# Kernel optimization log

Measured on AMD Instinct MI355X. Metric: run time of the kernel, lower is better.

Reference implementation:

```python
import jax, jax.numpy as jnp
import numpy as np

NUM_HEADS = 16
D_MODEL = 2048
DUPLICATES = 4
DEPTH = D_MODEL // NUM_HEADS  # 128
KV_HEADS = NUM_HEADS // DUPLICATES  # 4


def rope(x):
    # x: (b, s, d); RoPE over first 2*(d//2) dims (d even here), as in source
    b, s, d = x.shape
    dim = d // 2
    inv_freq = (10000.0 ** (-jnp.arange(0, dim, dtype=jnp.float32) / dim)).astype(x.dtype)
    pos = jnp.arange(s, dtype=x.dtype)[None, :, None]  # (1, s, 1)
    freqs = pos * inv_freq  # (1, s, dim)
    cos, sin = jnp.cos(freqs), jnp.sin(freqs)
    x1, x2 = x[..., :dim], x[..., dim:]
    return jnp.concatenate([x1 * cos - x2 * sin, x2 * cos + x1 * sin], axis=-1)


def setup_inputs() -> dict:
    key = jax.random.key(0)
    ks = jax.random.split(key, 6)
    b, s = 2, 2048
    x = jax.random.normal(ks[0], (b, s, D_MODEL), dtype=jnp.float32)
    mask = jnp.ones((b, 1, s, s), dtype=bool)
    std = 0.02
    Wq = jax.random.normal(ks[1], (D_MODEL, D_MODEL), dtype=jnp.float32) * std
    Wk = jax.random.normal(ks[2], (D_MODEL, D_MODEL // DUPLICATES), dtype=jnp.float32) * std
    Wv = jax.random.normal(ks[3], (D_MODEL, D_MODEL // DUPLICATES), dtype=jnp.float32) * std
    Wo = jax.random.normal(ks[4], (D_MODEL, D_MODEL), dtype=jnp.float32) * std
    bo = jnp.zeros((1, 1, D_MODEL), dtype=jnp.float32)
    return {"x": x, "mask": mask, "Wq": Wq, "Wk": Wk, "Wv": Wv, "Wo": Wo, "bo": bo}


def reference(x, mask, Wq, Wk, Wv, Wo, bo):
    b, s, d = x.shape
    # QKV projections; RoPE applied on full projected vectors (as in source)
    q = rope(x @ Wq)          # (b, s, d_model)
    k = rope(x @ Wk)          # (b, s, d_model/dup)
    v = x @ Wv                # (b, s, d_model/dup)
    # split heads
    q = q.reshape(b, s, NUM_HEADS, DEPTH).transpose(0, 2, 1, 3)     # (b, H, s, depth)
    k = k.reshape(b, s, KV_HEADS, DEPTH).transpose(0, 2, 1, 3)      # (b, Hkv, s, depth)
    v = v.reshape(b, s, KV_HEADS, DEPTH).transpose(0, 2, 1, 3)
    # GQA repeat (jnp.repeat on head axis, matching source)
    k = jnp.repeat(k, DUPLICATES, axis=1)                            # (b, H, s, depth)
    v = jnp.repeat(v, DUPLICATES, axis=1)
    # scaled dot-product attention (chunking in source is a pure partition of q; math identical)
    logits = jnp.einsum('bhqd,bhkd->bhqk', q, k) / jnp.sqrt(jnp.asarray(DEPTH, x.dtype))
    logits = jnp.where(mask, logits, jnp.asarray(-1e9, x.dtype))
    attn = jax.nn.softmax(logits, axis=-1)
    out = jnp.einsum('bhqk,bhkd->bhqd', attn, v)                     # (b, H, s, depth)
    out = out.transpose(0, 2, 1, 3).reshape(b, s, d)
    return out @ Wo + bo
```

## Files before the change

kernel.cpp:

```cpp
#include <hip/hip_runtime.h>
#include <hip/hip_bf16.h>
#include <stdint.h>

#define NHEADS 16
#define KVHEADS 4
#define DEPTH 128
#define SEQ 2048
#define DM 2048
#define NQKV 3072
#define SCALE 0.08838834764831845f

using u16 = unsigned short;
using u32 = unsigned int;
using u64 = unsigned long long;
using bf16x8 = __attribute__((ext_vector_type(8))) __bf16;
using f32x4  = __attribute__((ext_vector_type(4))) float;
using f32x16 = __attribute__((ext_vector_type(16))) float;
using u32x4  = __attribute__((ext_vector_type(4))) u32;

__device__ __forceinline__ u16 bits(float f) {
  return __builtin_bit_cast(u16, (__bf16)f);
}
__device__ __forceinline__ u32 pk2(float a, float b) {
  return (u32)bits(a) | ((u32)bits(b) << 16);
}

__device__ __forceinline__ void gll16(const void* g, void* l) {
  __builtin_amdgcn_global_load_lds((const __attribute__((address_space(1))) void*)g,
                                   (__attribute__((address_space(3))) void*)l, 16, 0, 0);
}


__global__ void k_cvt_x(const float4* __restrict__ x, u16* __restrict__ o, int n4) {
  int i = blockIdx.x * 256 + threadIdx.x;
  if (i >= n4) return;
  float4 v = x[i];
  u64 pk = (u64)bits(v.x) | ((u64)bits(v.y) << 16) | ((u64)bits(v.z) << 32) | ((u64)bits(v.w) << 48);
  reinterpret_cast<u64*>(o)[i] = pk;
}

__global__ void k_transpose_w(const float* __restrict__ in, u16* __restrict__ out, int K, int N) {
  __shared__ float tile[32][33];
  int n0 = blockIdx.x * 32, k0 = blockIdx.y * 32;
  int tx = threadIdx.x, ty = threadIdx.y;
  for (int i = 0; i < 4; i++) tile[ty + i * 8][tx] = in[(size_t)(k0 + ty + i * 8) * N + n0 + tx];
  __syncthreads();
  for (int i = 0; i < 4; i++)
    out[(size_t)(n0 + ty + i * 8) * K + k0 + tx] = bits(tile[tx][ty + i * 8]);
}

__global__ void k_trig(float2* __restrict__ tab) {
  int idx = blockIdx.x * 256 + threadIdx.x;
  int s = idx >> 10, j = idx & 1023;
  float inv = expf((float)j * (-9.210340371976184f / 1024.f));
  float f = (float)s * inv;
  float sv, cv;
  sincosf(f, &sv, &cv);
  tab[idx] = make_float2(cv, sv);
}

__global__ void k_rope_q(const float* __restrict__ qkv, const float2* __restrict__ tab,
                         u16* __restrict__ Qh) {
  int idx = blockIdx.x * 256 + threadIdx.x;
  int col = idx & 2047;
  int row = idx >> 11;
  int s = row & 2047;
  const float* base = qkv + (size_t)row * NQKV;
  float v = base[col], out;
  if (col < 1024) {
    float2 cs = tab[s * 1024 + col];
    out = v * cs.x - base[col + 1024] * cs.y;
  } else {
    int j = col - 1024;
    float2 cs = tab[s * 1024 + j];
    out = v * cs.x + base[col - 1024] * cs.y;
  }
  int h = col >> 7, d = col & 127;
  Qh[(((size_t)(row >> 11) * NHEADS + h) * SEQ + s) * DEPTH + d] = bits(out * SCALE);
}

__global__ void k_rope_k(const float* __restrict__ qkv, const float2* __restrict__ tab,
                         u16* __restrict__ Kh) {
  int idx = blockIdx.x * 256 + threadIdx.x;
  int col = idx & 511;
  int row = idx >> 9;
  int s = row & 2047;
  const float* base = qkv + (size_t)row * NQKV + 2048;
  float v = base[col], out;
  if (col < 256) {
    float2 cs = tab[s * 1024 + col * 4];
    out = v * cs.x - base[col + 256] * cs.y;
  } else {
    int j = col - 256;
    float2 cs = tab[s * 1024 + j * 4];
    out = v * cs.x + base[col - 256] * cs.y;
  }
  int h = col >> 7, d = col & 127;
  Kh[(((size_t)(row >> 11) * KVHEADS + h) * SEQ + s) * DEPTH + d] = bits(out);
}

__global__ void k_transpose_v(const float* __restrict__ qkv, u16* __restrict__ Vt) {
  __shared__ float tile[32][33];
  int gy = blockIdx.y;
  int d0 = (gy & 3) * 32, kvh = (gy >> 2) & 3, b = gy >> 4;
  int s0 = blockIdx.x * 32;
  int tx = threadIdx.x, ty = threadIdx.y;
  const float* base = qkv + (size_t)b * SEQ * NQKV + 2560 + kvh * 128 + d0;
  for (int i = 0; i < 4; i++)
    tile[ty + i * 8][tx] = base[(size_t)(s0 + ty + i * 8) * NQKV + tx];
  __syncthreads();
  u16* obase = Vt + (((size_t)b * KVHEADS + kvh) * DEPTH + d0) * SEQ;
  for (int i = 0; i < 4; i++)
    obase[(size_t)(ty + i * 8) * SEQ + s0 + tx] = bits(tile[tx][ty + i * 8]);
}

__global__ __launch_bounds__(256, 2) void k_gemm(const u16* __restrict__ A,
                                                 const u16* __restrict__ B,
                                                 float* __restrict__ C, int M, int N, int K,
                                                 const float* __restrict__ bias) {
  __shared__ u16 lA[128 * 32];
  __shared__ u16 lB[128 * 32];
  int nt = N >> 7;
  int nwg = gridDim.x;
  int bid = blockIdx.x;
  int swz = (bid & 7) * (nwg >> 3) + (bid >> 3);
  int bm = swz / nt, bn = swz % nt;
  int tid = threadIdx.x;
  int w = tid >> 6, l = tid & 63;
  int lr = l & 15, lg = l >> 4;
  int wr = w >> 1, wc = w & 1;
  f32x4 acc[4][4] = {};
  const u16* Abase = A + (size_t)(bm * 128) * K;
  const u16* Bbase = B + (size_t)(bn * 128) * K;
  for (int kt = 0; kt < K; kt += 32) {
    __syncthreads();
    for (int i = 0; i < 2; i++) {
      int c = w * 128 + i * 64 + l;
      int row = c >> 2, kc = c & 3;
      gll16(Abase + (size_t)row * K + kt + kc * 8, (char*)lA + (w * 128 + i * 64) * 16);
      gll16(Bbase + (size_t)row * K + kt + kc * 8, (char*)lB + (w * 128 + i * 64) * 16);
    }
    __syncthreads();
    bf16x8 a[4], bfr[4];
    for (int m = 0; m < 4; m++)
      a[m] = *reinterpret_cast<const bf16x8*>(&lA[(wr * 64 + m * 16 + lr) * 32 + lg * 8]);
    for (int n = 0; n < 4; n++)
      bfr[n] = *reinterpret_cast<const bf16x8*>(&lB[(wc * 64 + n * 16 + lr) * 32 + lg * 8]);
    for (int m = 0; m < 4; m++)
      for (int n = 0; n < 4; n++)
        acc[m][n] = __builtin_amdgcn_mfma_f32_16x16x32_bf16(a[m], bfr[n], acc[m][n], 0, 0, 0);
  }
  int r0 = bm * 128 + wr * 64, c0 = bn * 128 + wc * 64;
  for (int m = 0; m < 4; m++)
    for (int n = 0; n < 4; n++) {
      int col = c0 + n * 16 + lr;
      float bv = bias ? bias[col] : 0.f;
      for (int r = 0; r < 4; r++) {
        int row = r0 + m * 16 + lg * 4 + r;
        C[(size_t)row * N + col] = acc[m][n][r] + bv;
      }
    }
}

__global__ __launch_bounds__(512, 1) void k_attn(const u16* __restrict__ Qh,
                                                 const u16* __restrict__ Kh,
                                                 const u16* __restrict__ Vt,
                                                 u16* __restrict__ Ao) {
  __shared__ u16 lK[2][64 * 128];
  __shared__ u16 lV[2][128 * 64];
  __shared__ float lsc[8][32];

  int bid = blockIdx.x;
  int swz = (bid & 7) * 32 + (bid >> 3);
  int qt = swz & 7;
  int hd = (swz >> 3) & 3, kvh = (swz >> 5) & 3, b = swz >> 7;
  int h = kvh * 4 + hd;

  int tid = threadIdx.x;
  int w = tid >> 6, l = tid & 63;
  int hi = l >> 5;
  int q32 = l & 31;

  const u16* Kb = Kh + ((size_t)b * KVHEADS + kvh) * SEQ * DEPTH;
  const u16* Vb = Vt + ((size_t)b * KVHEADS + kvh) * DEPTH * SEQ;

  const u16* Qp = Qh + (((size_t)(b * NHEADS + h) * SEQ) + qt * 256 + w * 32 + q32) * DEPTH + hi * 8;
  bf16x8 qf[8];
#pragma unroll
  for (int ds = 0; ds < 8; ds++)
    qf[ds] = *reinterpret_cast<const bf16x8*>(Qp + ds * 16);

  f32x16 oacc[4] = {};
  float mrun = -INFINITY, lrun = 0.f;
  bool lo = (l < 32);

  {
#pragma unroll
    for (int i = 0; i < 2; i++) {
      int g = (w * 2 + i) * 64 + l;
      int kv = g >> 4, c = g & 15;
      gll16(Kb + (size_t)kv * DEPTH + ((c ^ (kv & 7)) << 3), (char*)lK[0] + (w * 2 + i) * 1024);
      int d = g >> 3, cv = g & 7;
      gll16(Vb + (size_t)d * SEQ + ((cv ^ (d & 7)) << 3), (char*)lV[0] + (w * 2 + i) * 1024);
    }
  }
  __syncthreads();

  int cur = 0;
  for (int t = 0; t < 32; t++) {
    if (t < 31) {
      int kv0 = (t + 1) * 64;
#pragma unroll
      for (int i = 0; i < 2; i++) {
        int g = (w * 2 + i) * 64 + l;
        int kv = g >> 4, c = g & 15;
        gll16(Kb + (size_t)(kv0 + kv) * DEPTH + ((c ^ (kv & 7)) << 3),
              (char*)lK[cur ^ 1] + (w * 2 + i) * 1024);
        int d = g >> 3, cv = g & 7;
        gll16(Vb + (size_t)d * SEQ + kv0 + ((cv ^ (d & 7)) << 3),
              (char*)lV[cur ^ 1] + (w * 2 + i) * 1024);
      }
    }

    const u16* lk = lK[cur];
    f32x16 sa[2] = {};
    __builtin_amdgcn_s_setprio(1);
#pragma unroll
    for (int ds = 0; ds < 8; ds++) {
#pragma unroll
      for (int a = 0; a < 2; a++) {
        int kv = a * 32 + q32;
        bf16x8 kf = *reinterpret_cast<const bf16x8*>(
            &lk[kv * DEPTH + (((ds * 2 + hi) ^ (kv & 7)) << 3)]);
        sa[a] = __builtin_amdgcn_mfma_f32_32x32x16_bf16(kf, qf[ds], sa[a], 0, 0, 0);
      }
    }
    __builtin_amdgcn_s_setprio(0);

    float pmax = sa[0][0];
#pragma unroll
    for (int r = 1; r < 16; r++) pmax = fmaxf(pmax, sa[0][r]);
#pragma unroll
    for (int r = 0; r < 16; r++) pmax = fmaxf(pmax, sa[1][r]);
    pmax = fmaxf(pmax, __shfl_xor(pmax, 32, 64));
    if (!__all(pmax - mrun <= 8.f)) {
      float mnew = fmaxf(mrun, pmax);
      float al = __expf(mrun - mnew);
      mrun = mnew;
      lrun *= al;
#pragma unroll
      for (int db = 0; db < 4; db++)
#pragma unroll
        for (int r = 0; r < 16; r++) oacc[db][r] *= al;
    }
    float ps = 0.f;
#pragma unroll
    for (int a = 0; a < 2; a++)
#pragma unroll
      for (int r = 0; r < 16; r++) {
        float p = __expf(sa[a][r] - mrun);
        sa[a][r] = p;
        ps += p;
      }
    ps += __shfl_xor(ps, 32, 64);
    lrun += ps;

    const u16* lv = lV[cur];
#pragma unroll
    for (int a = 0; a < 2; a++) {
#pragma unroll
      for (int js = 0; js < 2; js++) {
        int base = js * 8;
        u32 A0 = pk2(sa[a][base + 0], sa[a][base + 1]);
        u32 A1 = pk2(sa[a][base + 2], sa[a][base + 3]);
        u32 B0 = pk2(sa[a][base + 4], sa[a][base + 5]);
        u32 B1 = pk2(sa[a][base + 6], sa[a][base + 7]);
        u32 A0x = (u32)__shfl_xor((int)A0, 32, 64);
        u32 A1x = (u32)__shfl_xor((int)A1, 32, 64);
        u32 B0x = (u32)__shfl_xor((int)B0, 32, 64);
        u32 B1x = (u32)__shfl_xor((int)B1, 32, 64);
        u32x4 tw;
        tw.x = lo ? A0 : B0x;
        tw.y = lo ? A1 : B1x;
        tw.z = lo ? A0x : B0;
        tw.w = lo ? A1x : B1;
        bf16x8 pa = __builtin_bit_cast(bf16x8, tw);
        int ks = a * 2 + js;
        __builtin_amdgcn_s_setprio(1);
#pragma unroll
        for (int db = 0; db < 4; db++) {
          int d = db * 32 + q32;
          bf16x8 vf = *reinterpret_cast<const bf16x8*>(
              &lv[d * 64 + (((ks * 2 + hi) ^ (d & 7)) << 3)]);
          oacc[db] = __builtin_amdgcn_mfma_f32_32x32x16_bf16(pa, vf, oacc[db], 0, 0, 0);
        }
        __builtin_amdgcn_s_setprio(0);
      }
    }

    __syncthreads();
    cur ^= 1;
  }

  if (lo) lsc[w][q32] = 1.f / lrun;
  int q0 = qt * 256 + w * 32;
  u16* ob = Ao + (size_t)b * SEQ * DM + (size_t)h * DEPTH;
#pragma unroll
  for (int db = 0; db < 4; db++)
#pragma unroll
    for (int r = 0; r < 16; r++) {
      int row = (r & 3) + 8 * (r >> 2) + 4 * hi;
      ob[(size_t)(q0 + row) * DM + db * 32 + q32] = bits(oacc[db][r] * lsc[w][row]);
    }
}


extern "C" void kernel_launch(void* const* d_in, const int* in_sizes, int n_in,
                              void* d_out, int out_size, void* d_ws, size_t ws_size,
                              hipStream_t stream) {
  const float* x  = (const float*)d_in[0];
  const float* Wq = (const float*)d_in[2];
  const float* Wk = (const float*)d_in[3];
  const float* Wv = (const float*)d_in[4];
  const float* Wo = (const float*)d_in[5];
  const float* bo = (const float*)d_in[6];
  float* out = (float*)d_out;
  char* ws = (char*)d_ws;

  const size_t OFF_XB  = 0;
  const size_t OFF_WT  = 16777216;
  const size_t OFF_WOT = 29360128;
  const size_t OFF_TAB = 37748736;
  const size_t OFF_QKV = 54525952;
  const size_t OFF_QH  = 104857600;
  const size_t OFF_KH  = 121634816;
  const size_t OFF_VT  = 125829120;
  const size_t OFF_AO  = OFF_QKV;

  u16*    xb    = (u16*)(ws + OFF_XB);
  u16*    wqkvT = (u16*)(ws + OFF_WT);
  u16*    woT   = (u16*)(ws + OFF_WOT);
  float2* tab   = (float2*)(ws + OFF_TAB);
  float*  qkv   = (float*)(ws + OFF_QKV);
  u16*    Qhh   = (u16*)(ws + OFF_QH);
  u16*    Khh   = (u16*)(ws + OFF_KH);
  u16*    Vtt   = (u16*)(ws + OFF_VT);
  u16*    Ao    = (u16*)(ws + OFF_AO);

  dim3 tb(32, 8);
  k_cvt_x<<<8192, 256, 0, stream>>>((const float4*)x, xb, 2097152);
  k_transpose_w<<<dim3(64, 64), tb, 0, stream>>>(Wq, wqkvT, 2048, 2048);
  k_transpose_w<<<dim3(16, 64), tb, 0, stream>>>(Wk, wqkvT + (size_t)2048 * 2048, 2048, 512);
  k_transpose_w<<<dim3(16, 64), tb, 0, stream>>>(Wv, wqkvT + (size_t)2560 * 2048, 2048, 512);
  k_transpose_w<<<dim3(64, 64), tb, 0, stream>>>(Wo, woT, 2048, 2048);
  k_trig<<<8192, 256, 0, stream>>>(tab);
  k_gemm<<<768, 256, 0, stream>>>(xb, wqkvT, qkv, 4096, 3072, 2048, nullptr);
  k_rope_q<<<32768, 256, 0, stream>>>(qkv, tab, Qhh);
  k_rope_k<<<8192, 256, 0, stream>>>(qkv, tab, Khh);
  k_transpose_v<<<dim3(64, 32), tb, 0, stream>>>(qkv, Vtt);
  k_attn<<<256, 512, 0, stream>>>(Qhh, Khh, Vtt, Ao);
  k_gemm<<<512, 256, 0, stream>>>(Ao, woT, out, 4096, 2048, 2048, bo);
}
```

Before: 389.5 us.

## Replace GEMM with 256x256 double-buffered pipelined kernel; retile attention and use permlane swap

New measurement: 415.4 us. +6.7%, slower.

```diff
diff --git a/kernel.cpp b/kernel.cpp
--- a/kernel.cpp
+++ b/kernel.cpp
@@ -114,13 +114,55 @@
     obase[(size_t)(ty + i * 8) * SEQ + s0 + tx] = bits(tile[tx][ty + i * 8]);
 }
 
-__global__ __launch_bounds__(256, 2) void k_gemm(const u16* __restrict__ A,
-                                                 const u16* __restrict__ B,
-                                                 float* __restrict__ C, int M, int N, int K,
-                                                 const float* __restrict__ bias) {
-  __shared__ u16 lA[128 * 32];
-  __shared__ u16 lB[128 * 32];
-  int nt = N >> 7;
+
+#define GBAR __builtin_amdgcn_s_barrier()
+
+#define GSTAGE(GBASE, LHALF, KT, ROWB) do {                                   \
+  _Pragma("unroll") for (int i_ = 0; i_ < 2; i_++) {                          \
+    int rl_ = (l >> 3) + w * 8 + i_ * 64;                                     \
+    int cs_ = (l & 7) ^ ((rl_ & 4) >> 1);                                     \
+    gll16((GBASE) + (size_t)((ROWB) + rl_) * K + (KT) * 64 + cs_ * 8,         \
+          (char*)(LHALF) + w * 1024 + i_ * 8192);                             \
+  }                                                                           \
+} while (0)
+
+#define LDA8(DB, MH) do {                                                     \
+  const char* pa_ = (const char*)lA[DB][wm];                                  \
+  _Pragma("unroll") for (int mi_ = 0; mi_ < 4; mi_++)                         \
+  _Pragma("unroll") for (int kk_ = 0; kk_ < 2; kk_++) {                       \
+    int row_ = (MH) * 64 + mi_ * 16 + lr;                                     \
+    af[mi_ * 2 + kk_] = *(const bf16x8*)(pa_ + row_ * 128 +                   \
+        (((kk_ * 4 + lg) ^ ((row_ & 4) >> 1)) * 16));                         \
+  }                                                                           \
+} while (0)
+
+#define LDB4(DB, NH) do {                                                     \
+  const char* pb_ = (const char*)lB[DB][wn >> 1];                             \
+  _Pragma("unroll") for (int ni_ = 0; ni_ < 2; ni_++)                         \
+  _Pragma("unroll") for (int kk_ = 0; kk_ < 2; kk_++) {                       \
+    int row_ = (wn & 1) * 64 + (NH) * 32 + ni_ * 16 + lr;                     \
+    bfr[ni_ * 2 + kk_] = *(const bf16x8*)(pb_ + row_ * 128 +                  \
+        (((kk_ * 4 + lg) ^ ((row_ & 4) >> 1)) * 16));                         \
+  }                                                                           \
+} while (0)
+
+#define PHASE_MFMA(MH, NH) do {                                               \
+  __builtin_amdgcn_s_setprio(1);                                             \
+  _Pragma("unroll") for (int mi_ = 0; mi_ < 4; mi_++)                         \
+  _Pragma("unroll") for (int ni_ = 0; ni_ < 2; ni_++)                         \
+  _Pragma("unroll") for (int kk_ = 0; kk_ < 2; kk_++)                         \
+    acc[MH][NH][mi_][ni_] = __builtin_amdgcn_mfma_f32_16x16x32_bf16(          \
+        af[mi_ * 2 + kk_], bfr[ni_ * 2 + kk_], acc[MH][NH][mi_][ni_], 0, 0, 0); \
+  __builtin_amdgcn_s_setprio(0);                                             \
+} while (0)
+
+__global__ __launch_bounds__(512, 2) void k_gemm256(const u16* __restrict__ A,
+                                                    const u16* __restrict__ B,
+                                                    float* __restrict__ C, int M, int N, int K,
+                                                    const float* __restrict__ bias) {
+  __shared__ __align__(16) u16 lA[2][2][128 * 64];
+  __shared__ __align__(16) u16 lB[2][2][128 * 64];
+  int nt = N >> 8;
   int nwg = gridDim.x;
   int bid = blockIdx.x;
   int swz = (bid & 7) * (nwg >> 3) + (bid >> 3);
@@ -128,52 +170,105 @@
   int tid = threadIdx.x;
   int w = tid >> 6, l = tid & 63;
   int lr = l & 15, lg = l >> 4;
-  int wr = w >> 1, wc = w & 1;
-  f32x4 acc[4][4] = {};
-  const u16* Abase = A + (size_t)(bm * 128) * K;
-  const u16* Bbase = B + (size_t)(bn * 128) * K;
-  for (int kt = 0; kt < K; kt += 32) {
-    __syncthreads();
-    for (int i = 0; i < 2; i++) {
-      int c = w * 128 + i * 64 + l;
-      int row = c >> 2, kc = c & 3;
-      gll16(Abase + (size_t)row * K + kt + kc * 8, (char*)lA + (w * 128 + i * 64) * 16);
-      gll16(Bbase + (size_t)row * K + kt + kc * 8, (char*)lB + (w * 128 + i * 64) * 16);
-    }
-    __syncthreads();
-    bf16x8 a[4], bfr[4];
-    for (int m = 0; m < 4; m++)
-      a[m] = *reinterpret_cast<const bf16x8*>(&lA[(wr * 64 + m * 16 + lr) * 32 + lg * 8]);
-    for (int n = 0; n < 4; n++)
-      bfr[n] = *reinterpret_cast<const bf16x8*>(&lB[(wc * 64 + n * 16 + lr) * 32 + lg * 8]);
-    for (int m = 0; m < 4; m++)
-      for (int n = 0; n < 4; n++)
-        acc[m][n] = __builtin_amdgcn_mfma_f32_16x16x32_bf16(a[m], bfr[n], acc[m][n], 0, 0, 0);
+  int wm = w >> 2, wn = w & 3;
+  const u16* Abase = A + (size_t)(bm * 256) * K;
+  const u16* Bbase = B + (size_t)(bn * 256) * K;
+  int NT = K >> 6;
+
+  f32x4 acc[2][2][4][2] = {};
+
+  GSTAGE(Abase, lA[0][0], 0, 0);
+  GSTAGE(Abase, lA[0][1], 0, 128);
+  GSTAGE(Bbase, lB[0][0], 0, 0);
+  GSTAGE(Bbase, lB[0][1], 0, 128);
+  GSTAGE(Abase, lA[1][0], 1, 0);
+  asm volatile("s_waitcnt vmcnt(2)" ::: "memory");
+  GBAR;
+
+  for (int j = 0; j < (NT >> 1); j++) {
+    int kt1 = 2 * j + 1;
+    int ktn0 = (2 * j + 2) & (NT - 1);
+    int ktn1 = (2 * j + 3) & (NT - 1);
+    bf16x8 af[8];
+    bf16x8 bfr[4];
+    LDA8(0, 0);
+    LDB4(0, 0);
+    GSTAGE(Abase, lA[1][1], kt1, 128);
+    GBAR;
+    PHASE_MFMA(0, 0);
+    GBAR;
+    LDB4(0, 1);
+    GSTAGE(Bbase, lB[1][0], kt1, 0);
+    GBAR;
+    PHASE_MFMA(0, 1);
+    GBAR;
+    LDA8(0, 1);
+    GSTAGE(Bbase, lB[1][1], kt1, 128);
+    GBAR;
+    PHASE_MFMA(1, 1);
+    GBAR;
+    LDB4(0, 0);
+    GSTAGE(Abase, lA[0][0], ktn0, 0);
+    asm volatile("s_waitcnt vmcnt(2)" ::: "memory");
+    GBAR;
+    PHASE_MFMA(1, 0);
+    GBAR;
+    LDA8(1, 0);
+    LDB4(1, 0);
+    GSTAGE(Abase, lA[0][1], ktn0, 128);
+    GBAR;
+    PHASE_MFMA(0, 0);
+    GBAR;
+    LDB4(1, 1);
+    GSTAGE(Bbase, lB[0][0], ktn0, 0);
+    GBAR;
+    PHASE_MFMA(0, 1);
+    GBAR;
+    LDA8(1, 1);
+    GSTAGE(Bbase, lB[0][1], ktn0, 128);
+    GBAR;
+    PHASE_MFMA(1, 1);
+    GBAR;
+    LDB4(1, 0);
+    GSTAGE(Abase, lA[1][0], ktn1, 0);
+    asm volatile("s_waitcnt vmcnt(2)" ::: "memory");
+    GBAR;
+    PHASE_MFMA(1, 0);
+    GBAR;
   }
-  int r0 = bm * 128 + wr * 64, c0 = bn * 128 + wc * 64;
-  for (int m = 0; m < 4; m++)
-    for (int n = 0; n < 4; n++) {
-      int col = c0 + n * 16 + lr;
-      float bv = bias ? bias[col] : 0.f;
-      for (int r = 0; r < 4; r++) {
-        int row = r0 + m * 16 + lg * 4 + r;
-        C[(size_t)row * N + col] = acc[m][n][r] + bv;
-      }
-    }
-}
-
-__global__ __launch_bounds__(512, 1) void k_attn(const u16* __restrict__ Qh,
+  asm volatile("s_waitcnt vmcnt(0)" ::: "memory");
+
+  int r0 = bm * 256 + wm * 128, c0 = bn * 256 + wn * 64;
+#pragma unroll
+  for (int mh = 0; mh < 2; mh++)
+#pragma unroll
+    for (int mi = 0; mi < 4; mi++)
+#pragma unroll
+      for (int nh = 0; nh < 2; nh++)
+#pragma unroll
+        for (int ni = 0; ni < 2; ni++) {
+          int col = c0 + nh * 32 + ni * 16 + lr;
+          float bv = bias ? bias[col] : 0.f;
+#pragma unroll
+          for (int r = 0; r < 4; r++) {
+            int row = r0 + mh * 64 + mi * 16 + lg * 4 + r;
+            C[(size_t)row * N + col] = acc[mh][nh][mi][ni][r] + bv;
+          }
+        }
+}
+
+__global__ __launch_bounds__(256, 2) void k_attn(const u16* __restrict__ Qh,
                                                  const u16* __restrict__ Kh,
                                                  const u16* __restrict__ Vt,
                                                  u16* __restrict__ Ao) {
   __shared__ u16 lK[2][64 * 128];
   __shared__ u16 lV[2][128 * 64];
-  __shared__ float lsc[8][32];
+  __shared__ float lsc[4][32];
 
   int bid = blockIdx.x;
-  int swz = (bid & 7) * 32 + (bid >> 3);
-  int qt = swz & 7;
-  int hd = (swz >> 3) & 3, kvh = (swz >> 5) & 3, b = swz >> 7;
+  int swz = (bid & 7) * 64 + (bid >> 3);
+  int qt = swz & 15;
+  int hd = (swz >> 4) & 3, kvh = (swz >> 6) & 3, b = swz >> 8;
   int h = kvh * 4 + hd;
 
   int tid = threadIdx.x;
@@ -184,7 +279,7 @@
   const u16* Kb = Kh + ((size_t)b * KVHEADS + kvh) * SEQ * DEPTH;
   const u16* Vb = Vt + ((size_t)b * KVHEADS + kvh) * DEPTH * SEQ;
 
-  const u16* Qp = Qh + (((size_t)(b * NHEADS + h) * SEQ) + qt * 256 + w * 32 + q32) * DEPTH + hi * 8;
+  const u16* Qp = Qh + (((size_t)(b * NHEADS + h) * SEQ) + qt * 128 + w * 32 + q32) * DEPTH + hi * 8;
   bf16x8 qf[8];
 #pragma unroll
   for (int ds = 0; ds < 8; ds++)
@@ -196,12 +291,12 @@
 
   {
 #pragma unroll
-    for (int i = 0; i < 2; i++) {
-      int g = (w * 2 + i) * 64 + l;
+    for (int i = 0; i < 4; i++) {
+      int g = (w * 4 + i) * 64 + l;
       int kv = g >> 4, c = g & 15;
-      gll16(Kb + (size_t)kv * DEPTH + ((c ^ (kv & 7)) << 3), (char*)lK[0] + (w * 2 + i) * 1024);
+      gll16(Kb + (size_t)kv * DEPTH + ((c ^ (kv & 7)) << 3), (char*)lK[0] + (w * 4 + i) * 1024);
       int d = g >> 3, cv = g & 7;
-      gll16(Vb + (size_t)d * SEQ + ((cv ^ (d & 7)) << 3), (char*)lV[0] + (w * 2 + i) * 1024);
+      gll16(Vb + (size_t)d * SEQ + ((cv ^ (d & 7)) << 3), (char*)lV[0] + (w * 4 + i) * 1024);
     }
   }
   __syncthreads();
@@ -211,14 +306,14 @@
     if (t < 31) {
       int kv0 = (t + 1) * 64;
 #pragma unroll
-      for (int i = 0; i < 2; i++) {
-        int g = (w * 2 + i) * 64 + l;
+      for (int i = 0; i < 4; i++) {
+        int g = (w * 4 + i) * 64 + l;
         int kv = g >> 4, c = g & 15;
         gll16(Kb + (size_t)(kv0 + kv) * DEPTH + ((c ^ (kv & 7)) << 3),
-              (char*)lK[cur ^ 1] + (w * 2 + i) * 1024);
+              (char*)lK[cur ^ 1] + (w * 4 + i) * 1024);
         int d = g >> 3, cv = g & 7;
         gll16(Vb + (size_t)d * SEQ + kv0 + ((cv ^ (d & 7)) << 3),
-              (char*)lV[cur ^ 1] + (w * 2 + i) * 1024);
+              (char*)lV[cur ^ 1] + (w * 4 + i) * 1024);
       }
     }
 
@@ -275,15 +370,13 @@
         u32 A1 = pk2(sa[a][base + 2], sa[a][base + 3]);
         u32 B0 = pk2(sa[a][base + 4], sa[a][base + 5]);
         u32 B1 = pk2(sa[a][base + 6], sa[a][base + 7]);
-        u32 A0x = (u32)__shfl_xor((int)A0, 32, 64);
-        u32 A1x = (u32)__shfl_xor((int)A1, 32, 64);
-        u32 B0x = (u32)__shfl_xor((int)B0, 32, 64);
-        u32 B1x = (u32)__shfl_xor((int)B1, 32, 64);
+        asm volatile("v_permlane32_swap_b32 %0, %1" : "+v"(A0), "+v"(B0));
+        asm volatile("v_permlane32_swap_b32 %0, %1" : "+v"(A1), "+v"(B1));
         u32x4 tw;
-        tw.x = lo ? A0 : B0x;
-        tw.y = lo ? A1 : B1x;
-        tw.z = lo ? A0x : B0;
-        tw.w = lo ? A1x : B1;
+        tw.x = A0;
+        tw.y = A1;
+        tw.z = B0;
+        tw.w = B1;
         bf16x8 pa = __builtin_bit_cast(bf16x8, tw);
         int ks = a * 2 + js;
         __builtin_amdgcn_s_setprio(1);
@@ -303,7 +396,7 @@
   }
 
   if (lo) lsc[w][q32] = 1.f / lrun;
-  int q0 = qt * 256 + w * 32;
+  int q0 = qt * 128 + w * 32;
   u16* ob = Ao + (size_t)b * SEQ * DM + (size_t)h * DEPTH;
 #pragma unroll
   for (int db = 0; db < 4; db++)
@@ -354,10 +447,10 @@
   k_transpose_w<<<dim3(16, 64), tb, 0, stream>>>(Wv, wqkvT + (size_t)2560 * 2048, 2048, 512);
   k_transpose_w<<<dim3(64, 64), tb, 0, stream>>>(Wo, woT, 2048, 2048);
   k_trig<<<8192, 256, 0, stream>>>(tab);
-  k_gemm<<<768, 256, 0, stream>>>(xb, wqkvT, qkv, 4096, 3072, 2048, nullptr);
+  k_gemm256<<<192, 512, 0, stream>>>(xb, wqkvT, qkv, 4096, 3072, 2048, nullptr);
   k_rope_q<<<32768, 256, 0, stream>>>(qkv, tab, Qhh);
   k_rope_k<<<8192, 256, 0, stream>>>(qkv, tab, Khh);
   k_transpose_v<<<dim3(64, 32), tb, 0, stream>>>(qkv, Vtt);
-  k_attn<<<256, 512, 0, stream>>>(Qhh, Khh, Vtt, Ao);
-  k_gemm<<<512, 256, 0, stream>>>(Ao, woT, out, 4096, 2048, 2048, bo);
-}
+  k_attn<<<512, 256, 0, stream>>>(Qhh, Khh, Vtt, Ao);
+  k_gemm256<<<128, 512, 0, stream>>>(Ao, woT, out, 4096, 2048, 2048, bo);
+}
```
